# Kernel optimization log

Hardware: AMD Instinct MI355X
Metric: run time of the kernel (lower is better)

Reference implementation:

```python
import jax, jax.numpy as jnp
import numpy as np

N = 6144      # num_nodes
E = 256       # embed_dim
H = 4         # num_heads
D = E // H    # head_dim
EPS_LN = 1e-5


def setup_inputs() -> dict:
    key = jax.random.key(0)
    ks = jax.random.split(key, 8)
    x = jax.random.normal(ks[0], (N, E), jnp.float32)
    adj = (jax.random.uniform(ks[1], (N, N)) < 0.01).astype(jnp.float32)
    adj = jnp.maximum(adj, jnp.eye(N, dtype=jnp.float32))
    s = 1.0 / np.sqrt(E)
    Wq = jax.random.normal(ks[2], (E, E), jnp.float32) * s
    Wk = jax.random.normal(ks[3], (E, E), jnp.float32) * s
    Wv = jax.random.normal(ks[4], (E, E), jnp.float32) * s
    Wo = jax.random.normal(ks[5], (E, E), jnp.float32) * s
    bq = jnp.zeros((E,), jnp.float32)
    bk = jnp.zeros((E,), jnp.float32)
    bv = jnp.zeros((E,), jnp.float32)
    bo = jnp.zeros((E,), jnp.float32)
    gamma = jnp.ones((E,), jnp.float32)
    beta = jnp.zeros((E,), jnp.float32)
    return {"embeddings": x, "adj_matrix": adj,
            "Wq": Wq, "bq": bq, "Wk": Wk, "bk": bk, "Wv": Wv, "bv": bv,
            "Wo": Wo, "bo": bo, "gamma": gamma, "beta": beta}


def reference(embeddings, adj_matrix, Wq, bq, Wk, bk, Wv, bv, Wo, bo, gamma, beta):
    n, e = embeddings.shape
    h, d = H, e // H
    # linear projections (torch nn.Linear: x @ W.T + b)
    Q = (embeddings @ Wq.T + bq).reshape(n, h, d)
    K = (embeddings @ Wk.T + bk).reshape(n, h, d)
    V = (embeddings @ Wv.T + bv).reshape(n, h, d)
    # per-head node-node attention scores [h, n, n]
    scores = jnp.einsum('nhd,mhd->hnm', Q, K) / np.sqrt(d)
    scores = jnp.where(adj_matrix[None, :, :] == 0, -jnp.inf, scores)
    attn = jax.nn.softmax(scores, axis=-1)  # [h, n, n]
    out = jnp.einsum('hnm,mhd->nhd', attn, V).reshape(n, e)
    out = out @ Wo.T + bo
    # residual + LayerNorm
    y = embeddings + out
    mu = jnp.mean(y, axis=-1, keepdims=True)
    var = jnp.var(y, axis=-1, keepdims=True)
    return (y - mu) * jax.lax.rsqrt(var + EPS_LN) * gamma + beta
```

## Files before the change

kernel.cpp:

```cpp
#include <hip/hip_runtime.h>
#include <hip/hip_fp16.h>
#include <math.h>

constexpr int kN  = 6144;
constexpr int kE  = 256;
constexpr int kD  = 64;
constexpr int CAP = 128;

typedef float    f32x4  __attribute__((ext_vector_type(4)));
typedef float    f32x2  __attribute__((ext_vector_type(2)));
typedef _Float16 half8  __attribute__((ext_vector_type(8)));

__global__ __launch_bounds__(256) void convert_h(
    const float* __restrict__ X,
    const float* __restrict__ Wq, const float* __restrict__ Wk,
    const float* __restrict__ Wv, const float* __restrict__ Wo,
    __half* __restrict__ Xh,
    __half* __restrict__ Wqh, __half* __restrict__ Wkh,
    __half* __restrict__ Wvh, __half* __restrict__ Woh)
{
    const int i = blockIdx.x * 256 + threadIdx.x;
    const float* src; __half* dst; int off;
    if      (i < 393216) { src = X;  dst = Xh;  off = i; }
    else if (i < 409600) { src = Wq; dst = Wqh; off = i - 393216; }
    else if (i < 425984) { src = Wk; dst = Wkh; off = i - 409600; }
    else if (i < 442368) { src = Wv; dst = Wvh; off = i - 425984; }
    else                 { src = Wo; dst = Woh; off = i - 442368; }
    const float4 v = ((const float4*)src)[off];
    const __half2 a = __float22half2_rn(make_float2(v.x, v.y));
    const __half2 b = __float22half2_rn(make_float2(v.z, v.w));
    ((__half2*)dst)[off * 2 + 0] = a;
    ((__half2*)dst)[off * 2 + 1] = b;
}

template <int OUT_FP8>
__device__ __forceinline__ void gemm_mfma(
    const __half* __restrict__ A, const __half* __restrict__ B,
    const float* __restrict__ bias, void* __restrict__ Cout,
    const int n0, const int c0)
{
    const int lane = threadIdx.x & 63;
    const int w    = threadIdx.x >> 6;
    const int ar   = n0 + w * 16 + (lane & 15);
    const int ko   = (lane >> 4) * 8;

    f32x4 acc[4] = {{0.f,0.f,0.f,0.f},{0.f,0.f,0.f,0.f},
                    {0.f,0.f,0.f,0.f},{0.f,0.f,0.f,0.f}};

#pragma unroll
    for (int kc = 0; kc < kE; kc += 32) {
        const half8 af = *(const half8*)(A + (size_t)ar * kE + kc + ko);
#pragma unroll
        for (int j = 0; j < 4; ++j) {
            const int c = c0 + j * 16 + (lane & 15);
            const half8 bf = *(const half8*)(B + (size_t)c * kE + kc + ko);
            acc[j] = __builtin_amdgcn_mfma_f32_16x16x32_f16(af, bf, acc[j], 0, 0, 0);
        }
    }

    const int orow = n0 + w * 16 + (lane >> 4) * 4;
    const int ocol = lane & 15;
#pragma unroll
    for (int j = 0; j < 4; ++j) {
        const int c = c0 + j * 16 + ocol;
        const float bi = bias[c];
#pragma unroll
        for (int r = 0; r < 4; ++r) {
            const float v = acc[j][r] + bi;
            if (OUT_FP8) {
                const int pk = __builtin_amdgcn_cvt_pk_fp8_f32(v, v, 0, false);
                ((unsigned char*)Cout)[(size_t)(orow + r) * kE + c] = (unsigned char)pk;
            } else {
                ((__half*)Cout)[(size_t)(orow + r) * kE + c] = __float2half(v);
            }
        }
    }
}

__global__ __launch_bounds__(256) void proj_csr(
    const __half* __restrict__ Xh,
    const __half* __restrict__ Wqh, const float* __restrict__ bq,
    const __half* __restrict__ Wkh, const float* __restrict__ bk,
    const __half* __restrict__ Wvh, const float* __restrict__ bv,
    __half* __restrict__ Q, unsigned char* __restrict__ K,
    unsigned char* __restrict__ V,
    const float* __restrict__ adj,
    int* __restrict__ csr_cnt, unsigned short* __restrict__ csr_col)
{
    if (blockIdx.x < kN / 4) {
        const int lane = threadIdx.x & 63;
        const int r    = blockIdx.x * 4 + (threadIdx.x >> 6);
        const float* arow = adj + (size_t)r * kN;
        unsigned short* out = csr_col + (size_t)r * CAP;
        int base = 0;
#pragma unroll 4
        for (int it = 0; it < kN / 256; ++it) {
            const int col = it * 256 + lane * 4;
            const f32x4 a = __builtin_nontemporal_load((const f32x4*)(arow + col));
            const unsigned long long m0 = __ballot(a[0] != 0.f);
            const unsigned long long m1 = __ballot(a[1] != 0.f);
            const unsigned long long m2 = __ballot(a[2] != 0.f);
            const unsigned long long m3 = __ballot(a[3] != 0.f);
            const int c0 = __popcll(m0), c1 = __popcll(m1);
            const int c2 = __popcll(m2), c3 = __popcll(m3);
            const unsigned long long below = (1ull << lane) - 1ull;
            const int p0 = __popcll(m0 & below);
            const int p1 = c0 + __popcll(m1 & below);
            const int p2 = c0 + c1 + __popcll(m2 & below);
            const int p3 = c0 + c1 + c2 + __popcll(m3 & below);
            if (a[0] != 0.f && base + p0 < CAP) out[base + p0] = (unsigned short)(col + 0);
            if (a[1] != 0.f && base + p1 < CAP) out[base + p1] = (unsigned short)(col + 1);
            if (a[2] != 0.f && base + p2 < CAP) out[base + p2] = (unsigned short)(col + 2);
            if (a[3] != 0.f && base + p3 < CAP) out[base + p3] = (unsigned short)(col + 3);
            base += c0 + c1 + c2 + c3;
        }
        if (lane == 0) csr_cnt[r] = (base < CAP) ? base : CAP;
    } else {
        const int b = blockIdx.x - kN / 4;
        const int m = b / 384;
        const int r = b % 384;
        const int n0 = (r >> 2) * 64, c0 = (r & 3) * 64;
        if (m == 0)      gemm_mfma<0>(Xh, Wqh, bq, Q, n0, c0);
        else if (m == 1) gemm_mfma<1>(Xh, Wkh, bk, K, n0, c0);
        else             gemm_mfma<1>(Xh, Wvh, bv, V, n0, c0);
    }
}

__global__ __launch_bounds__(256) void attn_csr(
    const int* __restrict__ csr_cnt, const unsigned short* __restrict__ csr_col,
    const __half* __restrict__ Qm,
    const unsigned char* __restrict__ Km,
    const unsigned char* __restrict__ Vm,
    __half* __restrict__ O)
{
    const int n    = blockIdx.x;
    const int t    = threadIdx.x;
    const int lane = t & 63;
    const int head = t >> 6;

    __shared__ int   nbr[CAP];
    __shared__ float q_lds[kE];
    __shared__ float p_lds[4][64];

    const int cnt = min(csr_cnt[n], CAP);
    if (t < CAP && t < cnt) nbr[t] = (int)csr_col[(size_t)n * CAP + t];
    q_lds[t] = __half2float(Qm[(size_t)n * kE + t]);
    __syncthreads();

    float m = -INFINITY, lsum = 0.f, oacc = 0.f;
    const unsigned char* Vh = Vm + head * kD;
    const int vp   = lane & ~1;
    const int vsel = lane & 1;

    for (int b0 = 0; b0 < cnt; b0 += 64) {
        const int  bcnt  = min(64, cnt - b0);
        const bool valid = lane < bcnt;
        const int  idx   = valid ? nbr[b0 + lane] : n;
        const uint4* krow = (const uint4*)(Km + (size_t)idx * kE + head * kD);
        uint4 kw[4];
#pragma unroll
        for (int i = 0; i < 4; ++i) kw[i] = krow[i];

        float s = 0.f;
#pragma unroll
        for (int i = 0; i < 4; ++i) {
            const uint wds[4] = {kw[i].x, kw[i].y, kw[i].z, kw[i].w};
#pragma unroll
            for (int j = 0; j < 4; ++j) {
                const f32x2 lo = __builtin_amdgcn_cvt_pk_f32_fp8((int)wds[j], false);
                const f32x2 hi = __builtin_amdgcn_cvt_pk_f32_fp8((int)wds[j], true);
                const float* qv = &q_lds[head * kD + i * 16 + j * 4];
                s += lo[0] * qv[0] + lo[1] * qv[1] + hi[0] * qv[2] + hi[1] * qv[3];
            }
        }
        s *= 0.125f;
        if (!valid) s = -INFINITY;

        float bmax = s;
#pragma unroll
        for (int o = 32; o >= 1; o >>= 1) bmax = fmaxf(bmax, __shfl_xor(bmax, o, 64));
        const float mnew  = fmaxf(m, bmax);
        const float scale = __expf(m - mnew);
        const float p     = valid ? __expf(s - mnew) : 0.f;
        float bsum = p;
#pragma unroll
        for (int o = 32; o >= 1; o >>= 1) bsum += __shfl_xor(bsum, o, 64);
        lsum = lsum * scale + bsum;
        m    = mnew;
        oacc *= scale;

        p_lds[head][lane] = p;
        __syncthreads();

        int l = 0;
        for (; l + 8 <= bcnt; l += 8) {
            float pv[8], vv[8];
#pragma unroll
            for (int u = 0; u < 8; ++u) {
                const int vrow = nbr[b0 + l + u];
                const int pair = *(const unsigned short*)(Vh + (size_t)vrow * kE + vp);
                const f32x2 two = __builtin_amdgcn_cvt_pk_f32_fp8(pair, false);
                vv[u] = two[vsel];
                pv[u] = p_lds[head][l + u];
            }
#pragma unroll
            for (int u = 0; u < 8; ++u) oacc += pv[u] * vv[u];
        }
        for (; l < bcnt; ++l) {
            const int vrow = nbr[b0 + l];
            const int pair = *(const unsigned short*)(Vh + (size_t)vrow * kE + vp);
            const f32x2 two = __builtin_amdgcn_cvt_pk_f32_fp8(pair, false);
            oacc += p_lds[head][l] * two[vsel];
        }
        __syncthreads();
    }

    O[(size_t)n * kE + head * kD + lane] = __float2half(oacc / lsum);
}

__global__ __launch_bounds__(256) void oproj_ln(
    const __half* __restrict__ A, const __half* __restrict__ Woh,
    const float* __restrict__ bo, const float* __restrict__ X,
    const float* __restrict__ gamma, const float* __restrict__ beta,
    float* __restrict__ Out)
{
    const int n0   = blockIdx.x * 16;
    const int t    = threadIdx.x;
    const int lane = t & 63;
    const int w    = t >> 6;
    const int ar   = n0 + (lane & 15);
    const int ko   = (lane >> 4) * 8;

    __shared__ float sm_s[4][16], sm_q[4][16];

    f32x4 acc[4] = {{0.f,0.f,0.f,0.f},{0.f,0.f,0.f,0.f},
                    {0.f,0.f,0.f,0.f},{0.f,0.f,0.f,0.f}};

#pragma unroll
    for (int kc = 0; kc < kE; kc += 32) {
        const half8 af = *(const half8*)(A + (size_t)ar * kE + kc + ko);
#pragma unroll
        for (int j = 0; j < 4; ++j) {
            const int c = w * 64 + j * 16 + (lane & 15);
            const half8 bf = *(const half8*)(Woh + (size_t)c * kE + kc + ko);
            acc[j] = __builtin_amdgcn_mfma_f32_16x16x32_f16(af, bf, acc[j], 0, 0, 0);
        }
    }

    const int orow = n0 + (lane >> 4) * 4;
    const int ocol = lane & 15;

#pragma unroll
    for (int j = 0; j < 4; ++j) {
        const int c = w * 64 + j * 16 + ocol;
        const float bi = bo[c];
#pragma unroll
        for (int r = 0; r < 4; ++r)
            acc[j][r] += bi + X[(size_t)(orow + r) * kE + c];
    }

#pragma unroll
    for (int r = 0; r < 4; ++r) {
        float s = 0.f, q = 0.f;
#pragma unroll
        for (int j = 0; j < 4; ++j) { s += acc[j][r]; q += acc[j][r] * acc[j][r]; }
#pragma unroll
        for (int o = 8; o >= 1; o >>= 1) {
            s += __shfl_xor(s, o, 64);
            q += __shfl_xor(q, o, 64);
        }
        if (ocol == 0) {
            sm_s[w][(lane >> 4) * 4 + r] = s;
            sm_q[w][(lane >> 4) * 4 + r] = q;
        }
    }
    __syncthreads();

    float mean[4], inv[4];
#pragma unroll
    for (int r = 0; r < 4; ++r) {
        const int row16 = (lane >> 4) * 4 + r;
        const float S  = sm_s[0][row16] + sm_s[1][row16] + sm_s[2][row16] + sm_s[3][row16];
        const float Qq = sm_q[0][row16] + sm_q[1][row16] + sm_q[2][row16] + sm_q[3][row16];
        mean[r] = S * (1.f / 256.f);
        const float var = Qq * (1.f / 256.f) - mean[r] * mean[r];
        inv[r] = rsqrtf(var + 1e-5f);
    }

#pragma unroll
    for (int j = 0; j < 4; ++j) {
        const int c = w * 64 + j * 16 + ocol;
        const float g  = gamma[c];
        const float be = beta[c];
#pragma unroll
        for (int r = 0; r < 4; ++r)
            Out[(size_t)(orow + r) * kE + c] = (acc[j][r] - mean[r]) * inv[r] * g + be;
    }
}

extern "C" void kernel_launch(void* const* d_in, const int* in_sizes, int n_in,
                              void* d_out, int out_size, void* d_ws, size_t ws_size,
                              hipStream_t stream)
{
    const float* x   = (const float*)d_in[0];
    const float* adj = (const float*)d_in[1];
    const float* Wq  = (const float*)d_in[2];
    const float* bq  = (const float*)d_in[3];
    const float* Wk  = (const float*)d_in[4];
    const float* bk  = (const float*)d_in[5];
    const float* Wv  = (const float*)d_in[6];
    const float* bv  = (const float*)d_in[7];
    const float* Wo  = (const float*)d_in[8];
    const float* bo  = (const float*)d_in[9];
    const float* gam = (const float*)d_in[10];
    const float* bet = (const float*)d_in[11];

    char* p = (char*)d_ws;
    int*            csr_cnt = (int*)p;            p += (size_t)kN * 4;
    unsigned short* csr_col = (unsigned short*)p; p += (size_t)kN * CAP * 2;
    __half*         Xh      = (__half*)p;         p += (size_t)kN * kE * 2;
    __half*         Wqh     = (__half*)p;         p += (size_t)kE * kE * 2;
    __half*         Wkh     = (__half*)p;         p += (size_t)kE * kE * 2;
    __half*         Wvh     = (__half*)p;         p += (size_t)kE * kE * 2;
    __half*         Woh     = (__half*)p;         p += (size_t)kE * kE * 2;
    __half*         Q       = (__half*)p;         p += (size_t)kN * kE * 2;
    unsigned char*  K       = (unsigned char*)p;  p += (size_t)kN * kE;
    unsigned char*  V       = (unsigned char*)p;  p += (size_t)kN * kE;
    float*          Y       = (float*)d_out;

    convert_h<<<1792, 256, 0, stream>>>(x, Wq, Wk, Wv, Wo, Xh, Wqh, Wkh, Wvh, Woh);
    proj_csr<<<kN / 4 + 3 * (kN / 64) * (kE / 64), 256, 0, stream>>>(
        Xh, Wqh, bq, Wkh, bk, Wvh, bv, Q, K, V, adj, csr_cnt, csr_col);
    attn_csr<<<kN, 256, 0, stream>>>(csr_cnt, csr_col, Q, K, V, Q);
    oproj_ln<<<kN / 16, 256, 0, stream>>>(Q, Woh, bo, x, gam, bet, Y);
}
```

Baseline: 114.0 us.

## Fuse adjacency scan into attention kernel, drop CSR workspace

The adjacency-row compaction moves out of the projection kernel and into the attention kernel. Each block now scans its own adj row, with the four waves each covering a quarter of it, and builds the neighbor list in LDS through a shared atomic counter. This removes the global CSR write/read round trip and leaves a pure projection-GEMM kernel. In exchange, the large adj read no longer overlaps with the GEMM work. Neighbor order now depends on the atomic ordering, which changes the floating-point summation order.

```diff
diff --git a/kernel.cpp b/kernel.cpp
--- a/kernel.cpp
+++ b/kernel.cpp
@@ -77,57 +77,24 @@
     }
 }
 
-__global__ __launch_bounds__(256) void proj_csr(
+__global__ __launch_bounds__(256) void proj3(
     const __half* __restrict__ Xh,
     const __half* __restrict__ Wqh, const float* __restrict__ bq,
     const __half* __restrict__ Wkh, const float* __restrict__ bk,
     const __half* __restrict__ Wvh, const float* __restrict__ bv,
     __half* __restrict__ Q, unsigned char* __restrict__ K,
-    unsigned char* __restrict__ V,
+    unsigned char* __restrict__ V)
+{
+    const int m = blockIdx.x / 384;
+    const int r = blockIdx.x % 384;
+    const int n0 = (r >> 2) * 64, c0 = (r & 3) * 64;
+    if (m == 0)      gemm_mfma<0>(Xh, Wqh, bq, Q, n0, c0);
+    else if (m == 1) gemm_mfma<1>(Xh, Wkh, bk, K, n0, c0);
+    else             gemm_mfma<1>(Xh, Wvh, bv, V, n0, c0);
+}
+
+__global__ __launch_bounds__(256) void attn_scan(
     const float* __restrict__ adj,
-    int* __restrict__ csr_cnt, unsigned short* __restrict__ csr_col)
-{
-    if (blockIdx.x < kN / 4) {
-        const int lane = threadIdx.x & 63;
-        const int r    = blockIdx.x * 4 + (threadIdx.x >> 6);
-        const float* arow = adj + (size_t)r * kN;
-        unsigned short* out = csr_col + (size_t)r * CAP;
-        int base = 0;
-#pragma unroll 4
-        for (int it = 0; it < kN / 256; ++it) {
-            const int col = it * 256 + lane * 4;
-            const f32x4 a = __builtin_nontemporal_load((const f32x4*)(arow + col));
-            const unsigned long long m0 = __ballot(a[0] != 0.f);
-            const unsigned long long m1 = __ballot(a[1] != 0.f);
-            const unsigned long long m2 = __ballot(a[2] != 0.f);
-            const unsigned long long m3 = __ballot(a[3] != 0.f);
-            const int c0 = __popcll(m0), c1 = __popcll(m1);
-            const int c2 = __popcll(m2), c3 = __popcll(m3);
-            const unsigned long long below = (1ull << lane) - 1ull;
-            const int p0 = __popcll(m0 & below);
-            const int p1 = c0 + __popcll(m1 & below);
-            const int p2 = c0 + c1 + __popcll(m2 & below);
-            const int p3 = c0 + c1 + c2 + __popcll(m3 & below);
-            if (a[0] != 0.f && base + p0 < CAP) out[base + p0] = (unsigned short)(col + 0);
-            if (a[1] != 0.f && base + p1 < CAP) out[base + p1] = (unsigned short)(col + 1);
-            if (a[2] != 0.f && base + p2 < CAP) out[base + p2] = (unsigned short)(col + 2);
-            if (a[3] != 0.f && base + p3 < CAP) out[base + p3] = (unsigned short)(col + 3);
-            base += c0 + c1 + c2 + c3;
-        }
-        if (lane == 0) csr_cnt[r] = (base < CAP) ? base : CAP;
-    } else {
-        const int b = blockIdx.x - kN / 4;
-        const int m = b / 384;
-        const int r = b % 384;
-        const int n0 = (r >> 2) * 64, c0 = (r & 3) * 64;
-        if (m == 0)      gemm_mfma<0>(Xh, Wqh, bq, Q, n0, c0);
-        else if (m == 1) gemm_mfma<1>(Xh, Wkh, bk, K, n0, c0);
-        else             gemm_mfma<1>(Xh, Wvh, bv, V, n0, c0);
-    }
-}
-
-__global__ __launch_bounds__(256) void attn_csr(
-    const int* __restrict__ csr_cnt, const unsigned short* __restrict__ csr_col,
     const __half* __restrict__ Qm,
     const unsigned char* __restrict__ Km,
     const unsigned char* __restrict__ Vm,
@@ -139,13 +106,41 @@
     const int head = t >> 6;
 
     __shared__ int   nbr[CAP];
+    __shared__ int   lcnt;
     __shared__ float q_lds[kE];
     __shared__ float p_lds[4][64];
 
-    const int cnt = min(csr_cnt[n], CAP);
-    if (t < CAP && t < cnt) nbr[t] = (int)csr_col[(size_t)n * CAP + t];
+    if (t == 0) lcnt = 0;
     q_lds[t] = __half2float(Qm[(size_t)n * kE + t]);
     __syncthreads();
+
+    const float* arow = adj + (size_t)n * kN;
+#pragma unroll
+    for (int it = 0; it < 6; ++it) {
+        const int col = head * 1536 + it * 256 + lane * 4;
+        const f32x4 a = __builtin_nontemporal_load((const f32x4*)(arow + col));
+        const unsigned long long m0 = __ballot(a[0] != 0.f);
+        const unsigned long long m1 = __ballot(a[1] != 0.f);
+        const unsigned long long m2 = __ballot(a[2] != 0.f);
+        const unsigned long long m3 = __ballot(a[3] != 0.f);
+        const int c0 = __popcll(m0), c1 = __popcll(m1);
+        const int c2 = __popcll(m2), c3 = __popcll(m3);
+        const int c  = c0 + c1 + c2 + c3;
+        int base = 0;
+        if (lane == 0 && c) base = atomicAdd(&lcnt, c);
+        base = __shfl(base, 0, 64);
+        const unsigned long long below = (1ull << lane) - 1ull;
+        const int p0 = __popcll(m0 & below);
+        const int p1 = c0 + __popcll(m1 & below);
+        const int p2 = c0 + c1 + __popcll(m2 & below);
+        const int p3 = c0 + c1 + c2 + __popcll(m3 & below);
+        if (a[0] != 0.f && base + p0 < CAP) nbr[base + p0] = col + 0;
+        if (a[1] != 0.f && base + p1 < CAP) nbr[base + p1] = col + 1;
+        if (a[2] != 0.f && base + p2 < CAP) nbr[base + p2] = col + 2;
+        if (a[3] != 0.f && base + p3 < CAP) nbr[base + p3] = col + 3;
+    }
+    __syncthreads();
+    const int cnt = min(lcnt, CAP);
 
     float m = -INFINITY, lsum = 0.f, oacc = 0.f;
     const unsigned char* Vh = Vm + head * kD;
@@ -316,21 +311,18 @@
     const float* bet = (const float*)d_in[11];
 
     char* p = (char*)d_ws;
-    int*            csr_cnt = (int*)p;            p += (size_t)kN * 4;
-    unsigned short* csr_col = (unsigned short*)p; p += (size_t)kN * CAP * 2;
-    __half*         Xh      = (__half*)p;         p += (size_t)kN * kE * 2;
-    __half*         Wqh     = (__half*)p;         p += (size_t)kE * kE * 2;
-    __half*         Wkh     = (__half*)p;         p += (size_t)kE * kE * 2;
-    __half*         Wvh     = (__half*)p;         p += (size_t)kE * kE * 2;
-    __half*         Woh     = (__half*)p;         p += (size_t)kE * kE * 2;
-    __half*         Q       = (__half*)p;         p += (size_t)kN * kE * 2;
-    unsigned char*  K       = (unsigned char*)p;  p += (size_t)kN * kE;
-    unsigned char*  V       = (unsigned char*)p;  p += (size_t)kN * kE;
-    float*          Y       = (float*)d_out;
+    __half*        Xh  = (__half*)p;        p += (size_t)kN * kE * 2;
+    __half*        Wqh = (__half*)p;        p += (size_t)kE * kE * 2;
+    __half*        Wkh = (__half*)p;        p += (size_t)kE * kE * 2;
+    __half*        Wvh = (__half*)p;        p += (size_t)kE * kE * 2;
+    __half*        Woh = (__half*)p;        p += (size_t)kE * kE * 2;
+    __half*        Q   = (__half*)p;        p += (size_t)kN * kE * 2;
+    unsigned char* K   = (unsigned char*)p; p += (size_t)kN * kE;
+    unsigned char* V   = (unsigned char*)p; p += (size_t)kN * kE;
+    float*         Y   = (float*)d_out;
 
     convert_h<<<1792, 256, 0, stream>>>(x, Wq, Wk, Wv, Wo, Xh, Wqh, Wkh, Wvh, Woh);
-    proj_csr<<<kN / 4 + 3 * (kN / 64) * (kE / 64), 256, 0, stream>>>(
-        Xh, Wqh, bq, Wkh, bk, Wvh, bv, Q, K, V, adj, csr_cnt, csr_col);
-    attn_csr<<<kN, 256, 0, stream>>>(csr_cnt, csr_col, Q, K, V, Q);
+    proj3<<<1152, 256, 0, stream>>>(Xh, Wqh, bq, Wkh, bk, Wvh, bv, Q, K, V);
+    attn_scan<<<kN, 256, 0, stream>>>(adj, Q, K, V, Q);
     oproj_ln<<<kN / 16, 256, 0, stream>>>(Q, Woh, bo, x, gam, bet, Y);
 }
```

Result: faster. 107.8 us (-5.5%).
